# Kernel optimization log

Hardware: AMD Instinct MI355X
Metric: run time of the kernel (lower is better)

## Reference

```python
import jax, jax.numpy as jnp
import numpy as np

NUM_NODES = 64      # nodes per graph (fixed, required by flatten/matricize)
B = 256             # number of graphs
N = B * NUM_NODES   # total nodes
DEG = 16            # out-degree per node
E = N * DEG         # total edges
IN_C, OUT_C, HEADS, EDGE_DIM = 128, 64, 4, 16
NEG_SLOPE = 0.2     # PyG GATv2 leaky_relu slope


def setup_inputs() -> dict:
    key = jax.random.key(0)
    ks = jax.random.split(key, 10)
    x = jax.random.normal(ks[0], (N, IN_C), jnp.float32)
    # within-graph random edges: each node has DEG incoming edges
    dst = jnp.repeat(jnp.arange(N), DEG)
    src = (dst // NUM_NODES) * NUM_NODES + jax.random.randint(ks[1], (E,), 0, NUM_NODES)
    edge_index = jnp.stack([src, dst]).astype(jnp.int64)
    edge_attr = jax.random.normal(ks[2], (E, EDGE_DIM), jnp.float32)
    batch = (jnp.arange(N) // NUM_NODES).astype(jnp.int64)
    s = 0.1
    W_l = jax.random.normal(ks[3], (IN_C, HEADS * OUT_C), jnp.float32) * s
    W_r = jax.random.normal(ks[4], (IN_C, HEADS * OUT_C), jnp.float32) * s
    W_e = jax.random.normal(ks[5], (EDGE_DIM, HEADS * OUT_C), jnp.float32) * s
    att = jax.random.normal(ks[6], (HEADS, OUT_C), jnp.float32) * s
    b_gat = jax.random.normal(ks[7], (HEADS * OUT_C,), jnp.float32) * s
    lin_W = jax.random.normal(ks[8], (NUM_NODES * HEADS * OUT_C, NUM_NODES * OUT_C), jnp.float32) * 0.02
    lin_b = jax.random.normal(ks[9], (NUM_NODES * OUT_C,), jnp.float32) * 0.02
    return {"x": x, "edge_index": edge_index, "edge_attr": edge_attr, "batch": batch,
            "W_l": W_l, "W_r": W_r, "W_e": W_e, "att": att, "b_gat": b_gat,
            "lin_W": lin_W, "lin_b": lin_b}


def _gatv2(x, edge_index, edge_attr, W_l, W_r, W_e, att, b_gat):
    n = x.shape[0]
    src, dst = edge_index[0], edge_index[1]
    # add self loops (PyG default), edge_attr fill_value='mean'
    loop = jnp.arange(n)
    src = jnp.concatenate([src, loop])
    dst = jnp.concatenate([dst, loop])
    mean_ea = jnp.broadcast_to(edge_attr.mean(0, keepdims=True), (n, edge_attr.shape[1]))
    ea = jnp.concatenate([edge_attr, mean_ea], axis=0)
    H, C = att.shape
    xl = (x @ W_l).reshape(n, H, C)   # source transform
    xr = (x @ W_r).reshape(n, H, C)   # target transform
    ee = (ea @ W_e).reshape(-1, H, C)
    feat = xl[src] + xr[dst] + ee                              # [E+N, H, C]
    logits = jnp.einsum('ehc,hc->eh', jax.nn.leaky_relu(feat, NEG_SLOPE), att)
    # segment softmax over incoming edges of each dst node
    seg_max = jax.ops.segment_max(logits, dst, num_segments=n)
    ex = jnp.exp(logits - seg_max[dst])
    denom = jax.ops.segment_sum(ex, dst, num_segments=n)
    alpha = ex / denom[dst]                                    # [E+N, H]
    msg = alpha[:, :, None] * xl[src]                          # [E+N, H, C]
    summed = jax.ops.segment_sum(msg, dst, num_segments=n)
    # aggr='mean': average the weighted messages over neighbors
    cnt = jax.ops.segment_sum(jnp.ones((dst.shape[0],), x.dtype), dst, num_segments=n)
    out = summed / cnt[:, None, None]
    return out.reshape(n, H * C) + b_gat


def reference(x, edge_index, edge_attr, batch, W_l, W_r, W_e, att, b_gat, lin_W, lin_b):
    h = _gatv2(x, edge_index, edge_attr, W_l, W_r, W_e, att, b_gat)  # [N, H*C]
    # flatten: [B, num_nodes*H*C] (batch is sorted, fixed nodes per graph)
    h = h.reshape(B, NUM_NODES * HEADS * OUT_C)
    y = h @ lin_W + lin_b                                            # [B, num_nodes*C]
    # matricize back to node-major layout
    return y.reshape(-1, OUT_C)                                      # [N, C]
```

## Files before the change

kernel.cpp:

```cpp
#include <hip/hip_runtime.h>
#include <hip/hip_bf16.h>

#define N_NODES   16384
#define DEG       16
#define EDGES     262144
#define HC        256
#define KDIM      16384
#define NEG_SLOPE 0.2f

typedef __attribute__((ext_vector_type(8))) short short8;
typedef __attribute__((ext_vector_type(4))) float floatx4;

static __device__ __forceinline__ unsigned short f2bf(float f) {
    union { __hip_bfloat16 h; unsigned short u; } c;
    c.h = __float2bfloat16(f);
    return c.u;
}
static __device__ __forceinline__ unsigned int packbf2(float lo, float hi) {
    union { __hip_bfloat162 h2; unsigned int u; } c;
    c.h2 = __float22bfloat162_rn(make_float2(lo, hi));
    return c.u;
}

template <int CTRL>
static __device__ __forceinline__ float dpp_add(float v) {
    int x = __builtin_amdgcn_update_dpp(0, __float_as_int(v), CTRL, 0xF, 0xF, true);
    return v + __int_as_float(x);
}

__global__ __launch_bounds__(256) void k_ea_part(const float* __restrict__ ea,
                                                 float* __restrict__ part) {
    __shared__ float s[256];
    int b = blockIdx.x, t = threadIdx.x;
    int col = t & 15, r0 = t >> 4;
    const float* base = ea + (size_t)b * 1024 * 16;
    float acc = 0.f;
    for (int r = r0; r < 1024; r += 16) acc += base[r * 16 + col];
    s[t] = acc; __syncthreads();
    for (int off = 128; off >= 16; off >>= 1) {
        if (t < off) s[t] += s[t + off];
        __syncthreads();
    }
    if (t < 16) part[b * 16 + t] = s[t];
}

__global__ __launch_bounds__(256, 4) void k_attn(const int* __restrict__ ei,
                                                 const float* __restrict__ ea,
                                                 const float* __restrict__ eapart,
                                                 const float* __restrict__ att,
                                                 const float* __restrict__ We,
                                                 const float* __restrict__ x,
                                                 const float* __restrict__ Wl,
                                                 const float* __restrict__ Wr,
                                                 const float* __restrict__ bg,
                                                 unsigned short* __restrict__ hb) {
    __shared__ float xlS[64][68];
    __shared__ float xrS[64][68];
    __shared__ __align__(16) char uni[5376];
    __shared__ float mean[16];
    __shared__ float eeselfS[64];

    float* lgS = (float*)uni;
    unsigned int* srcSu = (unsigned int*)(uni + 4352);
    unsigned char* srcSb = (unsigned char*)(uni + 4352);
    unsigned int* BsU = (unsigned int*)uni;
    float (*ps)[16] = (float(*)[16])uni;
    (void)srcSb;

    int t = threadIdx.x;
    int g = blockIdx.x & 255, h = blockIdx.x >> 8;
    int hc0 = h * 64;

    int wave = t >> 6, lane = t & 63;
    int q = lane >> 4, l15 = lane & 15, lk = lane >> 4;

    {
        int col = t & 15, bgi = t >> 4;
        float a = 0.f;
        #pragma unroll
        for (int i = 0; i < 16; ++i)
            a += eapart[(bgi + i * 16) * 16 + col];
        ps[bgi][col] = a;
        __syncthreads();
        if (t < 16) {
            float m = 0.f;
            #pragma unroll
            for (int i = 0; i < 16; ++i) m += ps[i][t];
            mean[t] = m * (1.f / (float)EDGES);
        }
        __syncthreads();
        if (t < 64) {
            float acc = 0.f;
            #pragma unroll
            for (int d = 0; d < 16; ++d) acc += mean[d] * We[d * 256 + hc0 + t];
            eeselfS[t] = acc;
        }
        __syncthreads();
    }

    {
        int wm = wave;
        const float* xrow = x + ((size_t)(g * 64 + wm * 16 + l15)) * 128 + lk * 8;
        floatx4 accL[4], accR[4];
        #pragma unroll
        for (int i = 0; i < 4; ++i) { accL[i] = (floatx4)(0.f); accR[i] = (floatx4)(0.f); }

        int bkp = t >> 4, bc4 = t & 15;

        for (int k0 = 0; k0 < 128; k0 += 32) {
            float4 xv0 = *(const float4*)(xrow + k0);
            float4 xv1 = *(const float4*)(xrow + k0 + 4);
            union { unsigned int u[4]; short8 v; } aa;
            aa.u[0] = packbf2(xv0.x, xv0.y);
            aa.u[1] = packbf2(xv0.z, xv0.w);
            aa.u[2] = packbf2(xv1.x, xv1.y);
            aa.u[3] = packbf2(xv1.z, xv1.w);
            short8 af = aa.v;

            #pragma unroll
            for (int side = 0; side < 2; ++side) {
                const float* Wsel = side ? Wr : Wl;
                __syncthreads();
                {
                    const float* wp = Wsel + (size_t)(k0 + 2 * bkp) * 256 + hc0 + bc4 * 4;
                    float4 r0 = *(const float4*)wp;
                    float4 r1 = *(const float4*)(wp + 256);
                    BsU[(bc4 * 4 + 0) * 18 + bkp] = packbf2(r0.x, r1.x);
                    BsU[(bc4 * 4 + 1) * 18 + bkp] = packbf2(r0.y, r1.y);
                    BsU[(bc4 * 4 + 2) * 18 + bkp] = packbf2(r0.z, r1.z);
                    BsU[(bc4 * 4 + 3) * 18 + bkp] = packbf2(r0.w, r1.w);
                }
                __syncthreads();
                #pragma unroll
                for (int ni = 0; ni < 4; ++ni) {
                    int nr = ni * 16 + l15;
                    union { uint2 u[2]; short8 v; } bb;
                    bb.u[0] = *(const uint2*)&BsU[nr * 18 + lk * 4];
                    bb.u[1] = *(const uint2*)&BsU[nr * 18 + lk * 4 + 2];
                    if (side == 0)
                        accL[ni] = __builtin_amdgcn_mfma_f32_16x16x32_bf16(af, bb.v, accL[ni], 0, 0, 0);
                    else
                        accR[ni] = __builtin_amdgcn_mfma_f32_16x16x32_bf16(af, bb.v, accR[ni], 0, 0, 0);
                }
            }
        }
        #pragma unroll
        for (int ni = 0; ni < 4; ++ni) {
            #pragma unroll
            for (int r = 0; r < 4; ++r) {
                int node = wm * 16 + lk * 4 + r;
                xlS[node][l15 * 4 + ni] = accL[ni][r];
                xrS[node][l15 * 4 + ni] = accR[ni][r];
            }
        }
    }
    __syncthreads();

    {
        int4 v = *(const int4*)(ei + (size_t)g * 1024 + t * 4);
        srcSu[t] = (unsigned int)(v.x & 63) | ((unsigned int)(v.y & 63) << 8) |
                   ((unsigned int)(v.z & 63) << 16) | ((unsigned int)(v.w & 63) << 24);
    }

    short8 wf[4];
    float  attv[4];
    #pragma unroll
    for (int nt = 0; nt < 4; ++nt) {
        attv[nt] = att[hc0 + nt * 16 + l15];
        if (q < 2) {
            const float* wp = We + (size_t)(q * 8) * 256 + hc0 + nt * 16 + l15;
            float w0 = wp[0*256], w1 = wp[1*256], w2 = wp[2*256], w3 = wp[3*256];
            float w4 = wp[4*256], w5 = wp[5*256], w6 = wp[6*256], w7 = wp[7*256];
            union { unsigned int u[4]; short8 v; } bb;
            bb.u[0] = packbf2(w0, w1);
            bb.u[1] = packbf2(w2, w3);
            bb.u[2] = packbf2(w4, w5);
            bb.u[3] = packbf2(w6, w7);
            wf[nt] = bb.v;
        } else {
            wf[nt] = (short8)0;
        }
    }
    __syncthreads();

    for (int b = wave; b < 16; b += 4) {
        short8 af[4];
        #pragma unroll
        for (int mt = 0; mt < 4; ++mt) {
            if (q < 2) {
                const float* ep = ea + ((size_t)(g * 1024 + b * 64 + mt * 16 + l15)) * 16 + q * 8;
                float4 v0 = *(const float4*)ep;
                float4 v1 = *(const float4*)(ep + 4);
                union { unsigned int u[4]; short8 v; } bb;
                bb.u[0] = packbf2(v0.x, v0.y);
                bb.u[1] = packbf2(v0.z, v0.w);
                bb.u[2] = packbf2(v1.x, v1.y);
                bb.u[3] = packbf2(v1.z, v1.w);
                af[mt] = bb.v;
            } else {
                af[mt] = (short8)0;
            }
        }
        floatx4 acc[4][4];
        #pragma unroll
        for (int mt = 0; mt < 4; ++mt)
            #pragma unroll
            for (int nt = 0; nt < 4; ++nt)
                acc[mt][nt] = __builtin_amdgcn_mfma_f32_16x16x32_bf16(af[mt], wf[nt], (floatx4)(0.f), 0, 0, 0);

        #pragma unroll
        for (int mt = 0; mt < 4; ++mt) {
            float4 xrv = *(const float4*)&xrS[b * 4 + mt][l15 * 4];
            unsigned int sw = srcSu[b * 16 + mt * 4 + q];
            int sr[4] = {(int)(sw & 255), (int)((sw >> 8) & 255),
                         (int)((sw >> 16) & 255), (int)(sw >> 24)};
            float lsum[4];
            #pragma unroll
            for (int r = 0; r < 4; ++r) {
                float4 xlv = *(const float4*)&xlS[sr[r]][l15 * 4];
                float f, acc_sum = 0.f;
                f = acc[mt][0][r] + xlv.x + xrv.x; f = fmaxf(f, NEG_SLOPE * f); acc_sum += f * attv[0];
                f = acc[mt][1][r] + xlv.y + xrv.y; f = fmaxf(f, NEG_SLOPE * f); acc_sum += f * attv[1];
                f = acc[mt][2][r] + xlv.z + xrv.z; f = fmaxf(f, NEG_SLOPE * f); acc_sum += f * attv[2];
                f = acc[mt][3][r] + xlv.w + xrv.w; f = fmaxf(f, NEG_SLOPE * f); acc_sum += f * attv[3];
                lsum[r] = acc_sum;
            }
            #pragma unroll
            for (int r = 0; r < 4; ++r) {
                float v = lsum[r];
                v = dpp_add<0x111>(v);
                v = dpp_add<0x112>(v);
                v = dpp_add<0x114>(v);
                v = dpp_add<0x118>(v);
                if (l15 == 15) lgS[b * 64 + mt * 16 + q * 4 + r] = v;
            }
        }
    }

    {
        int n = wave * 16 + l15;
        float sum = 0.f;
        #pragma unroll
        for (int i = 0; i < 4; ++i) {
            float4 ev = *(const float4*)&eeselfS[q * 16 + i * 4];
            float4 av = *(const float4*)(att + hc0 + q * 16 + i * 4);
            #pragma unroll
            for (int j = 0; j < 4; ++j) {
                int p = (i * 4 + j) * 4 + q;
                float e = (j == 0) ? ev.x : (j == 1) ? ev.y : (j == 2) ? ev.z : ev.w;
                float a = (j == 0) ? av.x : (j == 1) ? av.y : (j == 2) ? av.z : av.w;
                float f = xlS[n][p] + xrS[n][p] + e;
                f = fmaxf(f, NEG_SLOPE * f);
                sum += f * a;
            }
        }
        sum += __shfl_xor(sum, 16);
        sum += __shfl_xor(sum, 32);
        if (q == 0) lgS[1024 + n] = sum;
    }
    __syncthreads();

    if (t < 64) {
        float lg[17];
        #pragma unroll
        for (int j = 0; j < 16; ++j) lg[j] = lgS[t * 16 + j];
        lg[16] = lgS[1024 + t];
        float m = lg[0];
        #pragma unroll
        for (int j = 1; j < 17; ++j) m = fmaxf(m, lg[j]);
        float ex[17], ssum = 0.f;
        #pragma unroll
        for (int j = 0; j < 17; ++j) { ex[j] = __expf(lg[j] - m); ssum += ex[j]; }
        float inv = 1.f / (17.f * ssum);
        #pragma unroll
        for (int j = 0; j < 16; ++j) lgS[t * 16 + j] = ex[j] * inv;
        lgS[1024 + t] = ex[16] * inv;
    }
    __syncthreads();

    {
        int c = lane;
        int pc = (c & 15) * 4 + (c >> 4);
        float bgv = bg[hc0 + c];
        for (int n = wave * 16; n < wave * 16 + 16; ++n) {
            float4 al0 = *(const float4*)&lgS[n * 16];
            float4 al1 = *(const float4*)&lgS[n * 16 + 4];
            float4 al2 = *(const float4*)&lgS[n * 16 + 8];
            float4 al3 = *(const float4*)&lgS[n * 16 + 12];
            unsigned int w0 = srcSu[n * 4 + 0], w1 = srcSu[n * 4 + 1];
            unsigned int w2 = srcSu[n * 4 + 2], w3 = srcSu[n * 4 + 3];
            float a0 = lgS[1024 + n] * xlS[n][pc];
            float a1 = 0.f;
            a0 += al0.x * xlS[w0 & 255][pc];        a1 += al0.y * xlS[(w0 >> 8) & 255][pc];
            a0 += al0.z * xlS[(w0 >> 16) & 255][pc]; a1 += al0.w * xlS[w0 >> 24][pc];
            a0 += al1.x * xlS[w1 & 255][pc];        a1 += al1.y * xlS[(w1 >> 8) & 255][pc];
            a0 += al1.z * xlS[(w1 >> 16) & 255][pc]; a1 += al1.w * xlS[w1 >> 24][pc];
            a0 += al2.x * xlS[w2 & 255][pc];        a1 += al2.y * xlS[(w2 >> 8) & 255][pc];
            a0 += al2.z * xlS[(w2 >> 16) & 255][pc]; a1 += al2.w * xlS[w2 >> 24][pc];
            a0 += al3.x * xlS[w3 & 255][pc];        a1 += al3.y * xlS[(w3 >> 8) & 255][pc];
            a0 += al3.z * xlS[(w3 >> 16) & 255][pc]; a1 += al3.w * xlS[w3 >> 24][pc];
            float val = a0 + a1 + bgv;
            hb[((size_t)(g * 64 + n)) * 256 + hc0 + c] = f2bf(val);
        }
    }
}

__global__ __launch_bounds__(256) void k_gemm(const unsigned short* __restrict__ hb,
                                              const float* __restrict__ W,
                                              float* __restrict__ parts) {
    __shared__ unsigned short As[3][256 * 32];
    __shared__ unsigned int   Bs[2][64][18];

    int t = threadIdx.x;
    int wave = t >> 6, lane = t & 63;
    int l15 = lane & 15, lk = lane >> 4;
    int bid = blockIdx.x;
    int s  = bid & 7;
    int n0 = (bid >> 3) * 64;
    int kbase = s * 2048;

    floatx4 acc[4][4];
    #pragma unroll
    for (int i = 0; i < 4; ++i)
        #pragma unroll
        for (int j = 0; j < 4; ++j)
            acc[i][j] = (floatx4)(0.f);

    int gc = ((lane & 3) - ((lane >> 3) & 3)) & 3;
    const unsigned short* a_src =
        hb + (size_t)(wave * 64 + (lane >> 2)) * KDIM + kbase + gc * 8;
    int ap_off[4];
    #pragma unroll
    for (int mi = 0; mi < 4; ++mi)
        ap_off[mi] = (wave * 64 + mi * 16 + l15) * 32 + (((lk + (l15 >> 1)) & 3) * 8);

    int bkp = t >> 4;
    int bc8 = t & 15;
    const float* b_src = W + (size_t)(kbase + 2 * bkp) * 4096 + n0 + bc8 * 4;

    #define ISSUE_A(step, buf)                                                   \
        {                                                                        \
            const unsigned short* gp_ = a_src + (size_t)(step) * 32;             \
            _Pragma("unroll")                                                    \
            for (int i_ = 0; i_ < 4; ++i_) {                                     \
                __builtin_amdgcn_global_load_lds(                                \
                    (const __attribute__((address_space(1))) unsigned int*)      \
                        (gp_ + (size_t)i_ * 16 * KDIM),                          \
                    (__attribute__((address_space(3))) unsigned int*)            \
                        &As[buf][(wave * 64 + i_ * 16) * 32],                    \
                    16, 0, 0);                                                   \
            }                                                                    \
        }
    #define LOAD_B(step, r0, r1)                                                 \
        {                                                                        \
            const float* wp_ = b_src + (size_t)(step) * 32 * 4096;               \
            r0 = *(const float4*)wp_;                                            \
            r1 = *(const float4*)(wp_ + 4096);                                   \
        }
    #define WRITE_B(buf, r0, r1)                                                 \
        {                                                                        \
            Bs[buf][bc8 * 4 + 0][bkp] = packbf2(r0.x, r1.x);                     \
            Bs[buf][bc8 * 4 + 1][bkp] = packbf2(r0.y, r1.y);                     \
            Bs[buf][bc8 * 4 + 2][bkp] = packbf2(r0.z, r1.z);                     \
            Bs[buf][bc8 * 4 + 3][bkp] = packbf2(r0.w, r1.w);                     \
        }
    #define COMPUTE(abuf, bbuf)                                                  \
        {                                                                        \
            short8 a_[4], b_[4];                                                 \
            _Pragma("unroll")                                                    \
            for (int mi = 0; mi < 4; ++mi)                                       \
                a_[mi] = *(const short8*)&As[abuf][ap_off[mi]];                  \
            _Pragma("unroll")                                                    \
            for (int ni = 0; ni < 4; ++ni) {                                     \
                int nr_ = ni * 16 + l15;                                         \
                union { uint2 u[2]; short8 v; } bb_;                             \
                bb_.u[0] = *(const uint2*)&Bs[bbuf][nr_][lk * 4];                \
                bb_.u[1] = *(const uint2*)&Bs[bbuf][nr_][lk * 4 + 2];            \
                b_[ni] = bb_.v;                                                  \
            }                                                                    \
            __builtin_amdgcn_s_setprio(1);                                       \
            _Pragma("unroll")                                                    \
            for (int mi = 0; mi < 4; ++mi)                                       \
                _Pragma("unroll")                                                \
                for (int ni = 0; ni < 4; ++ni)                                   \
                    acc[mi][ni] = __builtin_amdgcn_mfma_f32_16x16x32_bf16(       \
                        a_[mi], b_[ni], acc[mi][ni], 0, 0, 0);                   \
            __builtin_amdgcn_s_setprio(0);                                       \
        }
    #define VMCNT(n) __builtin_amdgcn_sched_barrier(0);                          \
                     asm volatile("s_waitcnt vmcnt(" #n ")" ::: "memory");       \
                     __builtin_amdgcn_sched_barrier(0)
    #define LGKM0    asm volatile("s_waitcnt lgkmcnt(0)" ::: "memory");          \
                     __builtin_amdgcn_sched_barrier(0)
    #define STEP(jA, abufI, jB, ldS0, ldS1, cA, cB, wB, wS0, wS1, VM)            \
        ISSUE_A(jA, abufI);                                                      \
        LOAD_B(jB, ldS0, ldS1);                                                  \
        COMPUTE(cA, cB);                                                         \
        VMCNT(VM);                                                               \
        WRITE_B(wB, wS0, wS1);                                                   \
        LGKM0;                                                                   \
        __builtin_amdgcn_s_barrier();

    float4 s0a, s0b, s1a, s1b, s2a, s2b;

    ISSUE_A(0, 0);
    LOAD_B(0, s0a, s0b);
    ISSUE_A(1, 1);
    LOAD_B(1, s1a, s1b);
    LOAD_B(2, s2a, s2b);
    VMCNT(8);
    WRITE_B(0, s0a, s0b);
    LGKM0;
    __builtin_amdgcn_s_barrier();

    for (int j = 0; j < 60; j += 6) {
        STEP(j + 2, 2, j + 3, s0a, s0b, 0, 0, 1, s1a, s1b, 8)
        STEP(j + 3, 0, j + 4, s1a, s1b, 1, 1, 0, s2a, s2b, 8)
        STEP(j + 4, 1, j + 5, s2a, s2b, 2, 0, 1, s0a, s0b, 8)
        STEP(j + 5, 2, j + 6, s0a, s0b, 0, 1, 0, s1a, s1b, 8)
        STEP(j + 6, 0, j + 7, s1a, s1b, 1, 0, 1, s2a, s2b, 8)
        STEP(j + 7, 1, j + 8, s2a, s2b, 2, 1, 0, s0a, s0b, 8)
    }
    STEP(62, 2, 63, s0a, s0b, 0, 0, 1, s1a, s1b, 8)
    ISSUE_A(63, 0);
    COMPUTE(1, 1);
    VMCNT(6);
    WRITE_B(0, s2a, s2b);
    LGKM0;
    __builtin_amdgcn_s_barrier();
    COMPUTE(2, 0);
    VMCNT(4);
    WRITE_B(1, s0a, s0b);
    LGKM0;
    __builtin_amdgcn_s_barrier();
    VMCNT(0);
    COMPUTE(0, 1);

    #undef ISSUE_A
    #undef LOAD_B
    #undef WRITE_B
    #undef COMPUTE
    #undef VMCNT
    #undef LGKM0
    #undef STEP

    float* dst = parts + (size_t)s * (256 * 4096);
    #pragma unroll
    for (int mi = 0; mi < 4; ++mi) {
        #pragma unroll
        for (int ni = 0; ni < 4; ++ni) {
            int col = n0 + ni * 16 + l15;
            #pragma unroll
            for (int r = 0; r < 4; ++r) {
                int row = wave * 64 + mi * 16 + lk * 4 + r;
                dst[(size_t)row * 4096 + col] = acc[mi][ni][r];
            }
        }
    }
}

__global__ __launch_bounds__(256) void k_reduce(const float* __restrict__ parts,
                                                const float* __restrict__ linb,
                                                float* __restrict__ out) {
    int idx = blockIdx.x * 256 + threadIdx.x;
    float v = linb[idx & 4095];
    #pragma unroll
    for (int s = 0; s < 8; ++s) v += parts[(size_t)s * (256 * 4096) + idx];
    out[idx] = v;
}

extern "C" void kernel_launch(void* const* d_in, const int* in_sizes, int n_in,
                              void* d_out, int out_size, void* d_ws, size_t ws_size,
                              hipStream_t stream) {
    (void)in_sizes; (void)n_in; (void)out_size; (void)ws_size;
    const float* x   = (const float*)d_in[0];
    const int*   ei  = (const int*)d_in[1];
    const float* ea  = (const float*)d_in[2];
    const float* Wl  = (const float*)d_in[4];
    const float* Wr  = (const float*)d_in[5];
    const float* We  = (const float*)d_in[6];
    const float* att = (const float*)d_in[7];
    const float* bg  = (const float*)d_in[8];
    const float* W   = (const float*)d_in[9];
    const float* lb  = (const float*)d_in[10];
    float* out = (float*)d_out;

    char* p = (char*)d_ws;
    unsigned short* hb  = (unsigned short*)p; p += 8388608;
    float* parts        = (float*)p;          p += 33554432;
    float* eapart       = (float*)p;          p += 16384;

    k_ea_part<<<256,  256, 0, stream>>>(ea, eapart);
    k_attn   <<<1024, 256, 0, stream>>>(ei, ea, eapart, att, We, x, Wl, Wr, bg, hb);
    k_gemm   <<<512,  256, 0, stream>>>(hb, W, parts);
    k_reduce <<<4096, 256, 0, stream>>>(parts, lb, out);
}
```

Baseline: 156.2 us.

## Fuse split-K reduction into GEMM via last-block atomic counter

Drops the separate reduce kernel. Each GEMM block now bumps a per-column-tile atomic counter after writing its partial result, and the last of the eight split-K blocks sums all partials plus bias into the output. The counters are zeroed in the first kernel. This saves one kernel launch and lets the reduction overlap with other GEMM blocks, at the cost of a serialized tail reduction done by only 64 blocks and extra fences and atomics.

```diff
diff --git a/kernel.cpp b/kernel.cpp
--- a/kernel.cpp
+++ b/kernel.cpp
@@ -29,9 +29,11 @@
 }
 
 __global__ __launch_bounds__(256) void k_ea_part(const float* __restrict__ ea,
-                                                 float* __restrict__ part) {
+                                                 float* __restrict__ part,
+                                                 int* __restrict__ cnt) {
     __shared__ float s[256];
     int b = blockIdx.x, t = threadIdx.x;
+    if (b == 0 && t < 64) cnt[t] = 0;
     int col = t & 15, r0 = t >> 4;
     const float* base = ea + (size_t)b * 1024 * 16;
     float acc = 0.f;
@@ -62,10 +64,8 @@
 
     float* lgS = (float*)uni;
     unsigned int* srcSu = (unsigned int*)(uni + 4352);
-    unsigned char* srcSb = (unsigned char*)(uni + 4352);
     unsigned int* BsU = (unsigned int*)uni;
     float (*ps)[16] = (float(*)[16])uni;
-    (void)srcSb;
 
     int t = threadIdx.x;
     int g = blockIdx.x & 255, h = blockIdx.x >> 8;
@@ -307,9 +307,13 @@
 
 __global__ __launch_bounds__(256) void k_gemm(const unsigned short* __restrict__ hb,
                                               const float* __restrict__ W,
-                                              float* __restrict__ parts) {
+                                              float* __restrict__ parts,
+                                              const float* __restrict__ lb,
+                                              float* __restrict__ out,
+                                              int* __restrict__ cnt) {
     __shared__ unsigned short As[3][256 * 32];
     __shared__ unsigned int   Bs[2][64][18];
+    __shared__ int lastFlag;
 
     int t = threadIdx.x;
     int wave = t >> 6, lane = t & 63;
@@ -457,16 +461,27 @@
             }
         }
     }
-}
-
-__global__ __launch_bounds__(256) void k_reduce(const float* __restrict__ parts,
-                                                const float* __restrict__ linb,
-                                                float* __restrict__ out) {
-    int idx = blockIdx.x * 256 + threadIdx.x;
-    float v = linb[idx & 4095];
-    #pragma unroll
-    for (int s = 0; s < 8; ++s) v += parts[(size_t)s * (256 * 4096) + idx];
-    out[idx] = v;
+
+    __threadfence();
+    if (t == 0) {
+        int old = __hip_atomic_fetch_add(&cnt[n0 >> 6], 1,
+                                         __ATOMIC_ACQ_REL, __HIP_MEMORY_SCOPE_AGENT);
+        lastFlag = (old == 7);
+    }
+    __syncthreads();
+    if (lastFlag) {
+        int c = t & 63;
+        int r0 = t >> 6;
+        float bias = lb[n0 + c];
+        for (int r = r0; r < 256; r += 4) {
+            size_t o = (size_t)r * 4096 + n0 + c;
+            float v = bias;
+            #pragma unroll
+            for (int s2 = 0; s2 < 8; ++s2)
+                v += parts[(size_t)s2 * (256 * 4096) + o];
+            out[o] = v;
+        }
+    }
 }
 
 extern "C" void kernel_launch(void* const* d_in, const int* in_sizes, int n_in,
@@ -489,9 +504,9 @@
     unsigned short* hb  = (unsigned short*)p; p += 8388608;
     float* parts        = (float*)p;          p += 33554432;
     float* eapart       = (float*)p;          p += 16384;
-
-    k_ea_part<<<256,  256, 0, stream>>>(ea, eapart);
+    int*   cnt          = (int*)p;            p += 1024;
+
+    k_ea_part<<<256,  256, 0, stream>>>(ea, eapart, cnt);
     k_attn   <<<1024, 256, 0, stream>>>(ei, ea, eapart, att, We, x, Wl, Wr, bg, hb);
-    k_gemm   <<<512,  256, 0, stream>>>(hb, W, parts);
-    k_reduce <<<4096, 256, 0, stream>>>(parts, lb, out);
-}
+    k_gemm   <<<512,  256, 0, stream>>>(hb, W, parts, lb, out, cnt);
+}
```

Result: slower. 250.5 us (+60.4%).
